# Kernel tuning notes

Hardware: AMD Instinct MI355X
Metric: run time of the kernel (lower is better)

## Reference

```python
import jax, jax.numpy as jnp
import numpy as np

EMBED_DIM = 64
N_EDGE_FEATURES = 16
NEG_SLOPE = 0.01  # torch LeakyReLU default


def setup_inputs() -> dict:
    key = jax.random.key(0)
    k1, k2, k3, k4 = jax.random.split(key, 4)
    B, N = 4, 512
    edge_features = jax.random.normal(k1, (B, N, N, N_EDGE_FEATURES), dtype=jnp.float32)
    adj = jax.random.uniform(k2, (B, N, N), dtype=jnp.float32)
    # torch Linear weight shape: (out_features, in_features); init ~ U(-1/sqrt(in), 1/sqrt(in))
    w4 = jax.random.uniform(k3, (EMBED_DIM, N_EDGE_FEATURES), dtype=jnp.float32,
                            minval=-1.0, maxval=1.0) / np.sqrt(N_EDGE_FEATURES)
    w3 = jax.random.uniform(k4, (EMBED_DIM, EMBED_DIM), dtype=jnp.float32,
                            minval=-1.0, maxval=1.0) / np.sqrt(EMBED_DIM)
    return {"edge_features": edge_features, "adj": adj, "w4": w4, "w3": w3}


def reference(edge_features, adj, w4, w3):
    # x4 = LeakyReLU(edge_features @ w4.T): (B, N, N, E)
    x4 = jnp.einsum('bijf,ef->bije', edge_features, w4)
    x4 = jnp.where(x4 >= 0, x4, NEG_SLOPE * x4)
    # adjacency-weighted sum over neighbor axis j: (B, N, E)
    summed = jnp.einsum('bij,bije->bie', adj, x4)
    # theta3: (B, N, E)
    return jnp.einsum('bie,oe->bio', summed, w3)
```

## Files before the change

kernel.cpp:

```cpp
#include <hip/hip_runtime.h>
#include <hip/hip_bf16.h>


typedef __attribute__((ext_vector_type(8))) short bf16x8;
typedef __attribute__((ext_vector_type(4))) float f32x4;
typedef __attribute__((ext_vector_type(4))) int   i32x4;

typedef __attribute__((address_space(1))) const unsigned int gu32;
typedef __attribute__((address_space(3))) unsigned int lu32;

constexpr int NN = 512;
constexpr int NF = 16;
constexpr int NE = 64;
constexpr int WAVES = 4;
constexpr int JT = 16;
constexpr int TPW = (NN / JT) / WAVES;
constexpr int TILEF = JT * NF;

__device__ __forceinline__ unsigned short f2bfu(float x) {
    return __builtin_bit_cast(unsigned short, __float2bfloat16(x));
}
__device__ __forceinline__ int pack2(float lo, float hi) {
    return (int)((unsigned)f2bfu(lo) | ((unsigned)f2bfu(hi) << 16));
}

__global__ void __launch_bounds__(256, 4)
edge_embed_kernel(const float* __restrict__ ef,
                  const float* __restrict__ adj,
                  const float* __restrict__ w4,
                  const float* __restrict__ w3,
                  float* __restrict__ out)
{
    const int row  = blockIdx.x;
    const int tid  = threadIdx.x;
    const int wave = tid >> 6;
    const int lane = tid & 63;
    const int m    = lane & 15;
    const int quad = lane >> 4;
    const int qb   = quad & 1;

    __shared__ float adjf[NN];
    __shared__ float stage[WAVES * TPW * TILEF];
    __shared__ float partial[WAVES * NE];
    __shared__ float summed[NE];

    const int j0 = wave * (TPW * JT);
    const int sbase = wave * (TPW * TILEF);

    const float2 a2 = *(const float2*)(adj + (size_t)row * NN + j0 + 2 * lane);

    float4 wf[8];
    #pragma unroll
    for (int g = 0; g < 4; ++g) {
        wf[2 * g]     = make_float4(0.f, 0.f, 0.f, 0.f);
        wf[2 * g + 1] = make_float4(0.f, 0.f, 0.f, 0.f);
        if (quad < 2) {
            const float* p = w4 + ((g * 16 + m) * NF + qb * 8);
            wf[2 * g]     = *(const float4*)p;
            wf[2 * g + 1] = *(const float4*)(p + 4);
        }
    }

    const float* efr = ef + (size_t)row * NN * NF;
    #pragma unroll
    for (int t = 0; t < TPW; ++t) {
        const float* gp = efr + (size_t)(j0 + t * JT) * NF + lane * 4;
        __builtin_amdgcn_global_load_lds((gu32*)gp, (lu32*)&stage[sbase + t * TILEF],
                                         16, 0, 0);
    }

    adjf[j0 + 2 * lane]     = a2.x;
    adjf[j0 + 2 * lane + 1] = a2.y;

    bf16x8 bfrag[4];
    #pragma unroll
    for (int g = 0; g < 4; ++g) {
        i32x4 v = {pack2(wf[2*g].x,   wf[2*g].y),
                   pack2(wf[2*g].z,   wf[2*g].w),
                   pack2(wf[2*g+1].x, wf[2*g+1].y),
                   pack2(wf[2*g+1].z, wf[2*g+1].w)};
        bfrag[g] = __builtin_bit_cast(bf16x8, v);
    }

    float accg[4] = {0.f, 0.f, 0.f, 0.f};

#define DO_TILE(T)                                                            \
    {                                                                         \
        __builtin_amdgcn_s_waitcnt(0x0F70 | (7 - (T)));       \
        const int sb = sbase + (T) * TILEF + m * 16 + qb * 8;                 \
        const float4 f0 = *(const float4*)&stage[sb];                         \
        const float4 f1 = *(const float4*)&stage[sb + 4];                     \
        i32x4 ai = {pack2(f0.x, f0.y), pack2(f0.z, f0.w),                     \
                    pack2(f1.x, f1.y), pack2(f1.z, f1.w)};                    \
        const bf16x8 a = __builtin_bit_cast(bf16x8, ai);                      \
        const float4 aj = *(const float4*)&adjf[j0 + (T) * JT + quad * 4];    \
        const float ajr[4] = {aj.x, aj.y, aj.z, aj.w};                        \
        const f32x4 zero = {0.f, 0.f, 0.f, 0.f};                              \
        _Pragma("unroll")                                                     \
        for (int g = 0; g < 4; ++g) {                                         \
            f32x4 d = __builtin_amdgcn_mfma_f32_16x16x32_bf16(a, bfrag[g],    \
                                                              zero, 0, 0, 0); \
            _Pragma("unroll")                                                 \
            for (int r = 0; r < 4; ++r) {                                     \
                float x = d[r];                                               \
                float v = fmaf(0.01f, fminf(x, 0.f), fmaxf(x, 0.f));          \
                accg[g] = fmaf(ajr[r], v, accg[g]);                           \
            }                                                                 \
        }                                                                     \
    }

    DO_TILE(0) DO_TILE(1) DO_TILE(2) DO_TILE(3)
    DO_TILE(4) DO_TILE(5) DO_TILE(6) DO_TILE(7)
#undef DO_TILE

    #pragma unroll
    for (int g = 0; g < 4; ++g) {
        accg[g] += __shfl_xor(accg[g], 16);
        accg[g] += __shfl_xor(accg[g], 32);
    }
    if (quad == 0) {
        #pragma unroll
        for (int g = 0; g < 4; ++g)
            partial[wave * NE + g * 16 + m] = accg[g];
    }
    __syncthreads();

    if (tid < NE)
        summed[tid] = partial[tid] + partial[NE + tid]
                    + partial[2 * NE + tid] + partial[3 * NE + tid];
    __syncthreads();

    if (wave == 0) {
        const float* w3r = w3 + lane * NE;
        float r = 0.f;
        #pragma unroll
        for (int e = 0; e < NE; e += 4) {
            float4 wv = *(const float4*)(w3r + e);
            float4 sv = *(const float4*)&summed[e];
            r = fmaf(wv.x, sv.x, r);
            r = fmaf(wv.y, sv.y, r);
            r = fmaf(wv.z, sv.z, r);
            r = fmaf(wv.w, sv.w, r);
        }
        out[(size_t)row * NE + lane] = r;
    }
}

extern "C" void kernel_launch(void* const* d_in, const int* in_sizes, int n_in,
                              void* d_out, int out_size, void* d_ws, size_t ws_size,
                              hipStream_t stream) {
    const float* ef  = (const float*)d_in[0];
    const float* adj = (const float*)d_in[1];
    const float* w4  = (const float*)d_in[2];
    const float* w3  = (const float*)d_in[3];
    float* out = (float*)d_out;

    const int rows = in_sizes[1] / NN;
    edge_embed_kernel<<<dim3(rows), dim3(256), 0, stream>>>(ef, adj, w4, w3, out);
}
```

Before: 105.4 us.

## Process two rows per block with in-place prefetch of second row's edge tiles

Measured after the change: 101.5 us. -3.6%, faster.

```diff
diff --git a/kernel.cpp b/kernel.cpp
--- a/kernel.cpp
+++ b/kernel.cpp
@@ -31,7 +31,8 @@
                   const float* __restrict__ w3,
                   float* __restrict__ out)
 {
-    const int row  = blockIdx.x;
+    const int row0 = blockIdx.x * 2;
+    const int row1 = row0 + 1;
     const int tid  = threadIdx.x;
     const int wave = tid >> 6;
     const int lane = tid & 63;
@@ -39,15 +40,15 @@
     const int quad = lane >> 4;
     const int qb   = quad & 1;
 
-    __shared__ float adjf[NN];
-    __shared__ float stage[WAVES * TPW * TILEF];
-    __shared__ float partial[WAVES * NE];
-    __shared__ float summed[NE];
+    __shared__ float stage[WAVES][TPW][TILEF];
+    __shared__ float adjw[WAVES][2][128];
+    __shared__ float partial[2][WAVES * NE];
+    __shared__ float summed[2][NE];
 
     const int j0 = wave * (TPW * JT);
-    const int sbase = wave * (TPW * TILEF);
 
-    const float2 a2 = *(const float2*)(adj + (size_t)row * NN + j0 + 2 * lane);
+    const float2 a20 = *(const float2*)(adj + (size_t)row0 * NN + j0 + 2 * lane);
+    const float2 a21 = *(const float2*)(adj + (size_t)row1 * NN + j0 + 2 * lane);
 
     float4 wf[8];
     #pragma unroll
@@ -61,16 +62,17 @@
         }
     }
 
-    const float* efr = ef + (size_t)row * NN * NF;
+    const float* efr0 = ef + (size_t)row0 * NN * NF;
+    const float* efr1 = ef + (size_t)row1 * NN * NF;
     #pragma unroll
     for (int t = 0; t < TPW; ++t) {
-        const float* gp = efr + (size_t)(j0 + t * JT) * NF + lane * 4;
-        __builtin_amdgcn_global_load_lds((gu32*)gp, (lu32*)&stage[sbase + t * TILEF],
+        const float* gp = efr0 + (size_t)(j0 + t * JT) * NF + lane * 4;
+        __builtin_amdgcn_global_load_lds((gu32*)gp, (lu32*)&stage[wave][t][0],
                                          16, 0, 0);
     }
 
-    adjf[j0 + 2 * lane]     = a2.x;
-    adjf[j0 + 2 * lane + 1] = a2.y;
+    *(float2*)&adjw[wave][0][2 * lane] = a20;
+    *(float2*)&adjw[wave][1][2 * lane] = a21;
 
     bf16x8 bfrag[4];
     #pragma unroll
@@ -82,18 +84,20 @@
         bfrag[g] = __builtin_bit_cast(bf16x8, v);
     }
 
-    float accg[4] = {0.f, 0.f, 0.f, 0.f};
+    float accg[2][4] = {{0.f,0.f,0.f,0.f},{0.f,0.f,0.f,0.f}};
 
 #define DO_TILE(T)                                                            \
     {                                                                         \
-        __builtin_amdgcn_s_waitcnt(0x0F70 | (7 - (T)));       \
-        const int sb = sbase + (T) * TILEF + m * 16 + qb * 8;                 \
-        const float4 f0 = *(const float4*)&stage[sb];                         \
-        const float4 f1 = *(const float4*)&stage[sb + 4];                     \
+        __builtin_amdgcn_s_waitcnt(0x0F70 | ((T) < 8 ? 7 : 15 - (T)));        \
+        const int r  = (T) >> 3;                               \
+        const int lt = (T) & 7;                   \
+        const float* sb = &stage[wave][lt][m * 16 + qb * 8];                  \
+        const float4 f0 = *(const float4*)sb;                                 \
+        const float4 f1 = *(const float4*)(sb + 4);                           \
         i32x4 ai = {pack2(f0.x, f0.y), pack2(f0.z, f0.w),                     \
                     pack2(f1.x, f1.y), pack2(f1.z, f1.w)};                    \
         const bf16x8 a = __builtin_bit_cast(bf16x8, ai);                      \
-        const float4 aj = *(const float4*)&adjf[j0 + (T) * JT + quad * 4];    \
+        const float4 aj = *(const float4*)&adjw[wave][r][lt * JT + quad * 4]; \
         const float ajr[4] = {aj.x, aj.y, aj.z, aj.w};                        \
         const f32x4 zero = {0.f, 0.f, 0.f, 0.f};                              \
         _Pragma("unroll")                                                     \
@@ -101,48 +105,62 @@
             f32x4 d = __builtin_amdgcn_mfma_f32_16x16x32_bf16(a, bfrag[g],    \
                                                               zero, 0, 0, 0); \
             _Pragma("unroll")                                                 \
-            for (int r = 0; r < 4; ++r) {                                     \
-                float x = d[r];                                               \
-                float v = fmaf(0.01f, fminf(x, 0.f), fmaxf(x, 0.f));          \
-                accg[g] = fmaf(ajr[r], v, accg[g]);                           \
+            for (int rr = 0; rr < 4; ++rr) {                                  \
+                float x = d[rr];                                              \
+                float v = fmaxf(x, 0.01f * x);                 \
+                accg[r][g] = fmaf(ajr[rr], v, accg[r][g]);                    \
             }                                                                 \
+        }                                                                     \
+        if ((T) < TPW) {           \
+            const float* gp = efr1 + (size_t)(j0 + lt * JT) * NF + lane * 4;  \
+            __builtin_amdgcn_global_load_lds((gu32*)gp,                       \
+                                             (lu32*)&stage[wave][lt][0],      \
+                                             16, 0, 0);                       \
         }                                                                     \
     }
 
-    DO_TILE(0) DO_TILE(1) DO_TILE(2) DO_TILE(3)
-    DO_TILE(4) DO_TILE(5) DO_TILE(6) DO_TILE(7)
+    DO_TILE(0)  DO_TILE(1)  DO_TILE(2)  DO_TILE(3)
+    DO_TILE(4)  DO_TILE(5)  DO_TILE(6)  DO_TILE(7)
+    DO_TILE(8)  DO_TILE(9)  DO_TILE(10) DO_TILE(11)
+    DO_TILE(12) DO_TILE(13) DO_TILE(14) DO_TILE(15)
 #undef DO_TILE
 
     #pragma unroll
-    for (int g = 0; g < 4; ++g) {
-        accg[g] += __shfl_xor(accg[g], 16);
-        accg[g] += __shfl_xor(accg[g], 32);
-    }
+    for (int r = 0; r < 2; ++r)
+        #pragma unroll
+        for (int g = 0; g < 4; ++g) {
+            accg[r][g] += __shfl_xor(accg[r][g], 16);
+            accg[r][g] += __shfl_xor(accg[r][g], 32);
+        }
     if (quad == 0) {
         #pragma unroll
-        for (int g = 0; g < 4; ++g)
-            partial[wave * NE + g * 16 + m] = accg[g];
+        for (int r = 0; r < 2; ++r)
+            #pragma unroll
+            for (int g = 0; g < 4; ++g)
+                partial[r][wave * NE + g * 16 + m] = accg[r][g];
     }
     __syncthreads();
 
-    if (tid < NE)
-        summed[tid] = partial[tid] + partial[NE + tid]
-                    + partial[2 * NE + tid] + partial[3 * NE + tid];
+    if (tid < 2 * NE) {
+        const int r = tid >> 6, e = tid & 63;
+        summed[r][e] = partial[r][e] + partial[r][NE + e]
+                     + partial[r][2 * NE + e] + partial[r][3 * NE + e];
+    }
     __syncthreads();
 
     if (wave == 0) {
         const float* w3r = w3 + lane * NE;
-        float r = 0.f;
+        float r0 = 0.f, r1 = 0.f;
         #pragma unroll
         for (int e = 0; e < NE; e += 4) {
             float4 wv = *(const float4*)(w3r + e);
-            float4 sv = *(const float4*)&summed[e];
-            r = fmaf(wv.x, sv.x, r);
-            r = fmaf(wv.y, sv.y, r);
-            r = fmaf(wv.z, sv.z, r);
-            r = fmaf(wv.w, sv.w, r);
+            float4 s0 = *(const float4*)&summed[0][e];
+            float4 s1 = *(const float4*)&summed[1][e];
+            r0 = fmaf(wv.x, s0.x, fmaf(wv.y, s0.y, fmaf(wv.z, s0.z, fmaf(wv.w, s0.w, r0))));
+            r1 = fmaf(wv.x, s1.x, fmaf(wv.y, s1.y, fmaf(wv.z, s1.z, fmaf(wv.w, s1.w, r1))));
         }
-        out[(size_t)row * NE + lane] = r;
+        out[(size_t)row0 * NE + lane] = r0;
+        out[(size_t)row1 * NE + lane] = r1;
     }
 }
 
@@ -156,5 +174,5 @@
     float* out = (float*)d_out;
 
     const int rows = in_sizes[1] / NN;
-    edge_embed_kernel<<<dim3(rows), dim3(256), 0, stream>>>(ef, adj, w4, w3, out);
+    edge_embed_kernel<<<dim3(rows / 2), dim3(256), 0, stream>>>(ef, adj, w4, w3, out);
 }
```
